# Optimization experiments

Hardware: AMD Instinct MI355X
Metric: run time of the kernel (lower is better)

## Reference

```python
import jax, jax.numpy as jnp
import numpy as np

SIGMA = 5.67e-8  # Stefan-Boltzmann constant
NX = 13
N = NX * NX  # 169 nodes
B = 131072


def _build_matrices(L=0.1, thickness=0.001, board_k=15.0, emis=0.8):
    dx = L / (NX - 1)
    dy = L / (NX - 1)
    GLx = thickness * board_k * dy / dx
    GLy = thickness * board_k * dx / dy
    GR = 2.0 * dx * dy * emis
    iface = {0, NX - 1, NX * NX - 1, NX * NX - NX}
    K = np.zeros((N, N), dtype=np.float32)
    for j in range(NX):
        for i in range(NX):
            idn = i + NX * j
            if idn in iface:
                K[idn, idn] = 1.0
            else:
                gii = 0.0
                if i + 1 < NX:
                    K[idn, idn + 1] = -GLx  # east
                    gii += GLx
                if i - 1 >= 0:
                    K[idn, idn - 1] = -GLx  # west
                    gii += GLx
                if j + 1 < NX:
                    K[idn, idn + NX] = -GLx  # north (original code uses -GLx here too)
                    gii += GLy
                if j - 1 >= 0:
                    K[idn, idn - NX] = -GLx  # south (original code uses -GLx here too)
                    gii += GLy
                K[idn, idn] = gii
    e = np.full(N, GR, dtype=np.float32)
    for t in iface:
        e[t] = 0.0
    return jnp.asarray(K), jnp.asarray(e)


def setup_inputs() -> dict:
    key = jax.random.key(0)
    k1, k2, k3, k4 = jax.random.split(key, 4)
    # realistic temperatures (K) and heat loads (W)
    outputs = 270.0 + 60.0 * jax.random.uniform(k1, (B, NX, NX), dtype=jnp.float32)
    heaters = 0.5 * jax.random.uniform(k2, (B, NX, NX), dtype=jnp.float32)
    interfaces = 0.5 * jax.random.uniform(k3, (B, NX, NX), dtype=jnp.float32)
    Tenv = 270.0 + 30.0 * jax.random.uniform(k4, (B, 1), dtype=jnp.float32)
    K, e_diag = _build_matrices()
    return {"outputs": outputs, "heaters": heaters, "interfaces": interfaces,
            "Tenv": Tenv, "K": K, "e_diag": e_diag}


def reference(outputs, heaters, interfaces, Tenv, K, e_diag):
    b = outputs.shape[0]
    T = outputs.reshape(b, -1)                    # [B, 169]
    Q = heaters.reshape(b, -1) + interfaces.reshape(b, -1)  # [B, 169]
    # original computes K @ T_nodes_x_batch; batch-major equivalent is T @ K^T
    conduction = jnp.einsum('bn,mn->bm', T, K)    # [B, 169]
    radiation = SIGMA * e_diag[None, :] * (T ** 4 - Tenv ** 4)  # Tenv [B,1] broadcasts
    excess = conduction + radiation - Q
    return jnp.mean(jnp.abs(excess))
```

## Files before the change

kernel.cpp:

```cpp
#include <hip/hip_runtime.h>
#include <math.h>


#define SIGMA_F 5.67e-8f

constexpr int BLOCK = 256;
constexpr int GRID  = 2048;

typedef float f4a __attribute__((ext_vector_type(4), aligned(4)));
typedef float f4b __attribute__((ext_vector_type(4), aligned(16)));

__global__ __launch_bounds__(256) void fused_residual_v2(
    const float* __restrict__ T,
    const float* __restrict__ H,
    const float* __restrict__ F,
    const float* __restrict__ Tenv,
    const float* __restrict__ K,
    const float* __restrict__ Ediag,
    float* __restrict__ partials,
    int total)
{
    __shared__ float sred[BLOCK / 64];

    const float GLx = -K[1 * 169 + 2];
    const float GRs = SIGMA_F * Ediag[1];

    const int lane = threadIdx.x & 63;
    float acc = 0.0f;

    const int gstride = GRID * BLOCK;
    for (int g = blockIdx.x * BLOCK + threadIdx.x; g * 4 < total; g += gstride) {
        const int e0 = g * 4;
        const int waveBase = e0 - lane * 4;
        const bool fast = (waveBase >= 16) && (waveBase + 64 * 4 + 16 <= total);

        if (fast) {
            f4b tc = *(const f4b*)(T + e0);
            f4a tm = *(const f4a*)(T + e0 - 13);
            f4a tp = *(const f4a*)(T + e0 + 13);
            f4b hv = *(const f4b*)(H + e0);
            f4b fv = *(const f4b*)(F + e0);

            float left = __shfl_up(tc.w, 1);
            if (lane == 0) left = T[e0 - 1];
            float right = __shfl_down(tc.x, 1);
            if (lane == 63) right = T[e0 + 4];

            unsigned ue = (unsigned)e0;
            unsigned b0 = ue / 169u;
            int m0 = (int)(ue - b0 * 169u);
            unsigned q13 = (unsigned)m0 / 13u;
            int i0 = m0 - (int)q13 * 13;

            float tvA = Tenv[b0];
            float tvB = tvA;
            if (m0 >= 166) tvB = Tenv[b0 + 1];
            float tv4A = (tvA * tvA) * (tvA * tvA);
            float tv4B = (tvB * tvB) * (tvB * tvB);

            const float tCv[4] = {tc.x, tc.y, tc.z, tc.w};
            const float tWv[4] = {left, tc.x, tc.y, tc.z};
            const float tEv[4] = {tc.y, tc.z, tc.w, right};
            const float tSv[4] = {tm.x, tm.y, tm.z, tm.w};
            const float tNv[4] = {tp.x, tp.y, tp.z, tp.w};
            const float hq[4]  = {hv.x + fv.x, hv.y + fv.y, hv.z + fv.z, hv.w + fv.w};

            int m = m0, ii = i0;
            bool wrapped = false;
            #pragma unroll
            for (int j = 0; j < 4; ++j) {
                float t = tCv[j];
                bool cE = (ii < 12), cW = (ii > 0), cN = (m < 156), cS = (m >= 13);
                bool ifc = (m == 0) | (m == 12) | (m == 156) | (m == 168);
                float s  = (cE ? tEv[j] : 0.0f) + (cW ? tWv[j] : 0.0f)
                         + (cN ? tNv[j] : 0.0f) + (cS ? tSv[j] : 0.0f);
                float nn = (cE ? 1.0f : 0.0f) + (cW ? 1.0f : 0.0f)
                         + (cN ? 1.0f : 0.0f) + (cS ? 1.0f : 0.0f);
                float t2 = t * t, t4 = t2 * t2;
                float tv4 = wrapped ? tv4B : tv4A;
                float ex = ifc ? (t - hq[j])
                               : (GLx * (nn * t - s) + GRs * (t4 - tv4) - hq[j]);
                acc += fabsf(ex);
                ++m; ++ii;
                if (ii == 13) ii = 0;
                if (m == 169) { m = 0; ii = 0; wrapped = true; }
            }
        } else {
            #pragma unroll
            for (int j = 0; j < 4; ++j) {
                int e = e0 + j;
                if (e >= total) break;
                unsigned b = (unsigned)e / 169u;
                int m = e - (int)b * 169;
                unsigned q13 = (unsigned)m / 13u;
                int ii = m - (int)q13 * 13;
                bool cE = (ii < 12), cW = (ii > 0), cN = (m < 156), cS = (m >= 13);
                bool ifc = (m == 0) | (m == 12) | (m == 156) | (m == 168);
                float t  = T[e];
                float tE = cE ? T[e + 1]  : 0.0f;
                float tW = cW ? T[e - 1]  : 0.0f;
                float tN = cN ? T[e + 13] : 0.0f;
                float tS = cS ? T[e - 13] : 0.0f;
                float s  = tE + tW + tN + tS;
                float nn = (float)((int)cE + (int)cW + (int)cN + (int)cS);
                float tv = Tenv[b];
                float tv4 = (tv * tv) * (tv * tv);
                float t2 = t * t, t4 = t2 * t2;
                float q = H[e] + F[e];
                float ex = ifc ? (t - q)
                               : (GLx * (nn * t - s) + GRs * (t4 - tv4) - q);
                acc += fabsf(ex);
            }
        }
    }

    #pragma unroll
    for (int off = 32; off > 0; off >>= 1)
        acc += __shfl_down(acc, off, 64);
    int wid = threadIdx.x >> 6;
    if (lane == 0) sred[wid] = acc;
    __syncthreads();
    if (threadIdx.x == 0) {
        float s = 0.0f;
        #pragma unroll
        for (int w = 0; w < BLOCK / 64; ++w) s += sred[w];
        partials[blockIdx.x] = s;
    }
}

__global__ __launch_bounds__(256) void finalize_kernel(
    const float* __restrict__ partials, int n,
    float* __restrict__ out, float inv_total)
{
    __shared__ float sred[BLOCK / 64];
    float acc = 0.0f;
    for (int i = (int)threadIdx.x; i < n; i += BLOCK) acc += partials[i];
    #pragma unroll
    for (int off = 32; off > 0; off >>= 1)
        acc += __shfl_down(acc, off, 64);
    int lane = threadIdx.x & 63;
    int wid  = threadIdx.x >> 6;
    if (lane == 0) sred[wid] = acc;
    __syncthreads();
    if (threadIdx.x == 0) {
        float s = 0.0f;
        #pragma unroll
        for (int w = 0; w < BLOCK / 64; ++w) s += sred[w];
        out[0] = s * inv_total;
    }
}

extern "C" void kernel_launch(void* const* d_in, const int* in_sizes, int n_in,
                              void* d_out, int out_size, void* d_ws, size_t ws_size,
                              hipStream_t stream) {
    const float* T    = (const float*)d_in[0];
    const float* H    = (const float*)d_in[1];
    const float* F    = (const float*)d_in[2];
    const float* Tenv = (const float*)d_in[3];
    const float* K    = (const float*)d_in[4];
    const float* E    = (const float*)d_in[5];
    float* out      = (float*)d_out;
    float* partials = (float*)d_ws;

    const int total = in_sizes[0];

    int grid = GRID;
    if ((size_t)grid * sizeof(float) > ws_size) grid = (int)(ws_size / sizeof(float));
    if (grid < 1) grid = 1;

    fused_residual_v2<<<grid, BLOCK, 0, stream>>>(T, H, F, Tenv, K, E, partials, total);

    const float inv_total = 1.0f / (float)total;
    finalize_kernel<<<1, BLOCK, 0, stream>>>(partials, grid, out, inv_total);
}
```

Baseline: 260.6 us.

## Process eight elements per thread with shuffle-based north/south neighbors and nontemporal loads

Each thread now handles eight consecutive elements instead of four. Because 8*2 is close to 13, most north/south neighbors can be taken by cross-lane shuffles from lanes one or two away, rather than through extra unaligned global loads. The heater and interface loads use nontemporal hints, and the grid is sized to cover the whole input once instead of using a fixed grid-stride count. The cost is more registers and shuffles per thread, plus a much larger partials array for the finalize kernel to reduce, which is bounded by the workspace size.

```diff
diff --git a/kernel.cpp b/kernel.cpp
--- a/kernel.cpp
+++ b/kernel.cpp
@@ -5,12 +5,11 @@
 #define SIGMA_F 5.67e-8f
 
 constexpr int BLOCK = 256;
-constexpr int GRID  = 2048;
 
 typedef float f4a __attribute__((ext_vector_type(4), aligned(4)));
 typedef float f4b __attribute__((ext_vector_type(4), aligned(16)));
 
-__global__ __launch_bounds__(256) void fused_residual_v2(
+__global__ __launch_bounds__(256) void fused_residual_v4(
     const float* __restrict__ T,
     const float* __restrict__ H,
     const float* __restrict__ F,
@@ -28,23 +27,54 @@
     const int lane = threadIdx.x & 63;
     float acc = 0.0f;
 
-    const int gstride = GRID * BLOCK;
-    for (int g = blockIdx.x * BLOCK + threadIdx.x; g * 4 < total; g += gstride) {
-        const int e0 = g * 4;
-        const int waveBase = e0 - lane * 4;
-        const bool fast = (waveBase >= 16) && (waveBase + 64 * 4 + 16 <= total);
+    const int gstride = gridDim.x * BLOCK;
+    for (int g = blockIdx.x * BLOCK + threadIdx.x; g * 8 < total; g += gstride) {
+        const int e0 = g * 8;
+        const int waveBase = e0 - lane * 8;
+        const bool fast = (waveBase >= 16) && (waveBase + 64 * 8 + 16 <= total);
 
         if (fast) {
-            f4b tc = *(const f4b*)(T + e0);
-            f4a tm = *(const f4a*)(T + e0 - 13);
-            f4a tp = *(const f4a*)(T + e0 + 13);
-            f4b hv = *(const f4b*)(H + e0);
-            f4b fv = *(const f4b*)(F + e0);
-
-            float left = __shfl_up(tc.w, 1);
+            f4b t0 = *(const f4b*)(T + e0);
+            f4b t1 = *(const f4b*)(T + e0 + 4);
+            f4b h0 = __builtin_nontemporal_load((const f4b*)(H + e0));
+            f4b h1 = __builtin_nontemporal_load((const f4b*)(H + e0 + 4));
+            f4b f0 = __builtin_nontemporal_load((const f4b*)(F + e0));
+            f4b f1 = __builtin_nontemporal_load((const f4b*)(F + e0 + 4));
+
+            float sv[8];
+            sv[0] = __shfl_up(t0.w, 2);
+            sv[1] = __shfl_up(t1.x, 2);
+            sv[2] = __shfl_up(t1.y, 2);
+            sv[3] = __shfl_up(t1.z, 2);
+            sv[4] = __shfl_up(t1.w, 2);
+            sv[5] = __shfl_up(t0.x, 1);
+            sv[6] = __shfl_up(t0.y, 1);
+            sv[7] = __shfl_up(t0.z, 1);
+            if (lane < 2) {
+                f4a a = *(const f4a*)(T + e0 - 13);
+                f4a b = *(const f4a*)(T + e0 - 9);
+                sv[0] = a.x; sv[1] = a.y; sv[2] = a.z; sv[3] = a.w;
+                sv[4] = b.x; sv[5] = b.y; sv[6] = b.z; sv[7] = b.w;
+            }
+            float nv[8];
+            nv[0] = __shfl_down(t1.y, 1);
+            nv[1] = __shfl_down(t1.z, 1);
+            nv[2] = __shfl_down(t1.w, 1);
+            nv[3] = __shfl_down(t0.x, 2);
+            nv[4] = __shfl_down(t0.y, 2);
+            nv[5] = __shfl_down(t0.z, 2);
+            nv[6] = __shfl_down(t0.w, 2);
+            nv[7] = __shfl_down(t1.x, 2);
+            if (lane >= 62) {
+                f4a a = *(const f4a*)(T + e0 + 13);
+                f4a b = *(const f4a*)(T + e0 + 17);
+                nv[0] = a.x; nv[1] = a.y; nv[2] = a.z; nv[3] = a.w;
+                nv[4] = b.x; nv[5] = b.y; nv[6] = b.z; nv[7] = b.w;
+            }
+            float left = __shfl_up(t1.w, 1);
             if (lane == 0) left = T[e0 - 1];
-            float right = __shfl_down(tc.x, 1);
-            if (lane == 63) right = T[e0 + 4];
+            float right = __shfl_down(t0.x, 1);
+            if (lane == 63) right = T[e0 + 8];
 
             unsigned ue = (unsigned)e0;
             unsigned b0 = ue / 169u;
@@ -54,26 +84,25 @@
 
             float tvA = Tenv[b0];
             float tvB = tvA;
-            if (m0 >= 166) tvB = Tenv[b0 + 1];
+            if (m0 >= 162) tvB = Tenv[b0 + 1];
             float tv4A = (tvA * tvA) * (tvA * tvA);
             float tv4B = (tvB * tvB) * (tvB * tvB);
 
-            const float tCv[4] = {tc.x, tc.y, tc.z, tc.w};
-            const float tWv[4] = {left, tc.x, tc.y, tc.z};
-            const float tEv[4] = {tc.y, tc.z, tc.w, right};
-            const float tSv[4] = {tm.x, tm.y, tm.z, tm.w};
-            const float tNv[4] = {tp.x, tp.y, tp.z, tp.w};
-            const float hq[4]  = {hv.x + fv.x, hv.y + fv.y, hv.z + fv.z, hv.w + fv.w};
+            const float tC[8] = {t0.x, t0.y, t0.z, t0.w, t1.x, t1.y, t1.z, t1.w};
+            const float tW[8] = {left, t0.x, t0.y, t0.z, t0.w, t1.x, t1.y, t1.z};
+            const float tE[8] = {t0.y, t0.z, t0.w, t1.x, t1.y, t1.z, t1.w, right};
+            const float hq[8] = {h0.x + f0.x, h0.y + f0.y, h0.z + f0.z, h0.w + f0.w,
+                                 h1.x + f1.x, h1.y + f1.y, h1.z + f1.z, h1.w + f1.w};
 
             int m = m0, ii = i0;
             bool wrapped = false;
             #pragma unroll
-            for (int j = 0; j < 4; ++j) {
-                float t = tCv[j];
+            for (int j = 0; j < 8; ++j) {
+                float t = tC[j];
                 bool cE = (ii < 12), cW = (ii > 0), cN = (m < 156), cS = (m >= 13);
                 bool ifc = (m == 0) | (m == 12) | (m == 156) | (m == 168);
-                float s  = (cE ? tEv[j] : 0.0f) + (cW ? tWv[j] : 0.0f)
-                         + (cN ? tNv[j] : 0.0f) + (cS ? tSv[j] : 0.0f);
+                float s  = (cE ? tE[j] : 0.0f) + (cW ? tW[j] : 0.0f)
+                         + (cN ? nv[j] : 0.0f) + (cS ? sv[j] : 0.0f);
                 float nn = (cE ? 1.0f : 0.0f) + (cW ? 1.0f : 0.0f)
                          + (cN ? 1.0f : 0.0f) + (cS ? 1.0f : 0.0f);
                 float t2 = t * t, t4 = t2 * t2;
@@ -87,7 +116,7 @@
             }
         } else {
             #pragma unroll
-            for (int j = 0; j < 4; ++j) {
+            for (int j = 0; j < 8; ++j) {
                 int e = e0 + j;
                 if (e >= total) break;
                 unsigned b = (unsigned)e / 169u;
@@ -97,11 +126,11 @@
                 bool cE = (ii < 12), cW = (ii > 0), cN = (m < 156), cS = (m >= 13);
                 bool ifc = (m == 0) | (m == 12) | (m == 156) | (m == 168);
                 float t  = T[e];
-                float tE = cE ? T[e + 1]  : 0.0f;
-                float tW = cW ? T[e - 1]  : 0.0f;
-                float tN = cN ? T[e + 13] : 0.0f;
-                float tS = cS ? T[e - 13] : 0.0f;
-                float s  = tE + tW + tN + tS;
+                float tEv = cE ? T[e + 1]  : 0.0f;
+                float tWv = cW ? T[e - 1]  : 0.0f;
+                float tNv = cN ? T[e + 13] : 0.0f;
+                float tSv = cS ? T[e - 13] : 0.0f;
+                float s  = tEv + tWv + tNv + tSv;
                 float nn = (float)((int)cE + (int)cW + (int)cN + (int)cS);
                 float tv = Tenv[b];
                 float tv4 = (tv * tv) * (tv * tv);
@@ -164,11 +193,11 @@
 
     const int total = in_sizes[0];
 
-    int grid = GRID;
+    int grid = (total / 8 + BLOCK - 1) / BLOCK;
     if ((size_t)grid * sizeof(float) > ws_size) grid = (int)(ws_size / sizeof(float));
     if (grid < 1) grid = 1;
 
-    fused_residual_v2<<<grid, BLOCK, 0, stream>>>(T, H, F, Tenv, K, E, partials, total);
+    fused_residual_v4<<<grid, BLOCK, 0, stream>>>(T, H, F, Tenv, K, E, partials, total);
 
     const float inv_total = 1.0f / (float)total;
     finalize_kernel<<<1, BLOCK, 0, stream>>>(partials, grid, out, inv_total);
```

Result: faster. 246.2 us (-5.5%).
